# Performance work log

Measured on AMD Instinct MI355X. Metric: run time of the kernel, lower is better.

## Reference

```python
import jax, jax.numpy as jnp
import numpy as np

B, S, H, D = 2, 512, 64, 64   # batch, seq_len, head_dim, d_v=d_k
DT = 0.01                      # uniform measurement time step
NU, DELTA, ETA = 0.5, 1.0, 1.0


def _cmat(k, dout, din, scale):
    kr, ki = jax.random.split(k)
    return jnp.stack([jax.random.normal(kr, (dout, din)),
                      jax.random.normal(ki, (dout, din))]) * scale


def _cmm(W, b, X):
    """Complex matmul + bias. W:(2,O,I), b:(2,O,1), X:(B,2,S,I) -> (B,2,S,O)."""
    Yr = X[:, 0] @ W[0].T - X[:, 1] @ W[1].T + b[0].T
    Yi = X[:, 0] @ W[1].T + X[:, 1] @ W[0].T + b[1].T
    return jnp.stack([Yr, Yi], axis=1)


def _chad(K, V):
    """Complex hadamard of kernel K:(2,Si,Sj,D) with V:(B,2,Sj,D) -> (B,2,Si,Sj,D)."""
    Vr, Vi = V[:, 0, None], V[:, 1, None]           # (B,1,Sj,D)
    return jnp.stack([K[0][None] * Vr - K[1][None] * Vi,
                      K[0][None] * Vi + K[1][None] * Vr], axis=1)


def setup_inputs() -> dict:
    key = jax.random.key(0)
    ks = jax.random.split(key, 20)
    sc = 1.0 / np.sqrt(2 * H)
    t = jnp.arange(S + 1, dtype=jnp.float32) * DT
    return {
        "X_q": jax.random.normal(ks[0], (B, 2, S, H), jnp.float32),
        "X_k": jax.random.normal(ks[1], (B, 2, S, H), jnp.float32),
        "X_v": jax.random.normal(ks[2], (B, 2, S, H), jnp.float32),
        "t_measure_all": jnp.tile(t[None], (B, 1)),
        "lambda1": jnp.stack([jax.random.normal(ks[3], (D // 2, 1)),
                              jax.random.normal(ks[4], (D // 2, 1))]),
        "lam_Omega_sqrt": jax.random.normal(ks[5], (1, D, 1)) / np.sqrt(D),
        "lam_Omega0_sqrt": jax.random.normal(ks[6], (1, D, 1)) / np.sqrt(D),
        "lam_Gamma_sqrt": jax.random.normal(ks[7], (1, D, 1)) / np.sqrt(D),
        "lam_C": jnp.ones((1, D, 1), jnp.float32),
        "W_q": _cmat(ks[8], D, H, sc), "W_k": _cmat(ks[9], D, H, sc),
        "W_v": _cmat(ks[10], D, H, sc), "W_p": _cmat(ks[11], H, D, sc),
        "W_e": _cmat(ks[12], H, D, sc),
        "b_q": _cmat(ks[13], D, 1, sc), "b_k": _cmat(ks[14], D, 1, sc),
        "b_v": _cmat(ks[15], D, 1, sc), "b_p": _cmat(ks[16], H, 1, sc),
        "b_e": _cmat(ks[17], H, 1, sc),
    }


def reference(X_q, X_k, X_v, t_measure_all, lambda1, lam_Omega_sqrt,
              lam_Omega0_sqrt, lam_Gamma_sqrt, lam_C, W_q, W_k, W_v, W_p, W_e,
              b_q, b_k, b_v, b_p, b_e):
    # Stable conjugate-pair eigenvalues lambda_h (real<0) from lambda1 (2, D/2, 1)
    lr = -jnp.abs(lambda1[0, :, 0])
    li = lambda1[1, :, 0]
    real = jnp.concatenate([lr, lr])        # (D,)
    imag = jnp.concatenate([li, -li])       # (D,)
    Om = (lam_Omega_sqrt ** 2)[0, :, 0]
    Om0 = (lam_Omega0_sqrt ** 2)[0, :, 0]
    Gam = (lam_Gamma_sqrt ** 2)[0, :, 0]
    C = lam_C[0, :, 0]

    # Complex QKV projections
    Q = _cmm(W_q, b_q, X_q)
    Kk = _cmm(W_k, b_k, X_k)
    V = _cmm(W_v, b_v, X_v)

    # Pairwise propagation kernel exp(lambda * (t_i - t_j))
    t = t_measure_all[0, :-1]                       # (S,)
    dt = t[:, None] - t[None, :]                    # (S,S)
    decay = jnp.exp(real * dt[:, :, None])
    ph = imag * dt[:, :, None]
    Kexp = jnp.stack([decay * jnp.cos(ph), decay * jnp.sin(ph)])  # (2,S,S,D)

    # Kalman steady-state precision: propagated variance + measurement noise
    exp2 = jnp.exp((2.0 * real) * jnp.abs(dt)[:, :, None])        # (S,S,D)
    var = exp2 * Om0 + Om * (exp2 - 1.0) / (2.0 * real)
    P = 1.0 / (C ** 2 * var + Gam)                                # (S,S,D)

    # Estimates (propagated values) and residuals (query vs propagated key)
    Xhat = _chad(Kexp, V)                           # (B,2,S,S,D)
    Khat = _chad(Kexp, Kk)
    R = Q[:, :, :, None, :] - C * Khat              # (B,2,S,S,D)

    maha = P * (R[:, 0] ** 2 + R[:, 1] ** 2)        # (B,S,S,D)
    denom = 1.0 + NU * jnp.sum(maha, axis=-1, keepdims=True)
    mask = jnp.tril(jnp.ones((S, S), X_q.dtype))[:, :, None]
    A = (P / denom) * mask
    Xhat = Xhat * mask
    Qij = A / jnp.sum(A, axis=2, keepdims=True)     # normalize over j
    est_v = jnp.sum(Qij[:, None] * Xhat, axis=3)    # (B,2,S,D)

    est = _cmm(W_e, b_e, est_v)

    # One-step prediction in eigenbasis
    dtl = t_measure_all[:, -1] - t_measure_all[:, -2]   # (B,)
    dr = jnp.exp(real * dtl[:, None])
    pph = imag * dtl[:, None]
    mr, mi = dr * jnp.cos(pph), dr * jnp.sin(pph)       # (B,D)
    pr = mr[:, None] * est_v[:, 0] - mi[:, None] * est_v[:, 1]
    pi = mr[:, None] * est_v[:, 1] + mi[:, None] * est_v[:, 0]
    pred = _cmm(W_p, b_p, jnp.stack([pr, pi], axis=1))

    out = DELTA * pred + ETA * est
    return (est, out, Qij, Xhat, jnp.stack([real, imag]))
```

## Files before the change

### kernel.cpp

```cpp
#include <hip/hip_runtime.h>
#include <math.h>

#define SQ 512
#define NU_C 0.5f

typedef float fvec4 __attribute__((ext_vector_type(4)));
typedef float fvec2 __attribute__((ext_vector_type(2)));

#define EST_OFF   0
#define OUT_OFF   131072
#define QIJ_OFF   262144
#define XHAT_OFF  33816576
#define LAM_OFF   100925440

#define WQ_OFF  0
#define WK_OFF  131072
#define WV_OFF  262144
#define WEV_OFF 393216

__global__ __launch_bounds__(256) void proj_kernel(
    const float* __restrict__ Xq, const float* __restrict__ Xk, const float* __restrict__ Xv,
    const float* __restrict__ Wq, const float* __restrict__ Wk, const float* __restrict__ Wv,
    const float* __restrict__ bq, const float* __restrict__ bk, const float* __restrict__ bv,
    float* __restrict__ ws)
{
    const int TILE = 16;
    __shared__ float WT0[64 * 65];
    __shared__ float WT1[64 * 65];
    __shared__ float XT[2 * TILE * 64];

    int t   = threadIdx.x;
    int blk = blockIdx.x;
    int p   = blk >> 6;
    int sub = blk & 63;
    int b   = sub >> 5;
    int s0  = (sub & 31) * TILE;

    const float* Xs[3]   = {Xq, Xk, Xv};
    const float* Wsrc[3] = {Wq, Wk, Wv};
    const float* bs[3]   = {bq, bk, bv};
    float* dst[3] = {ws + WQ_OFF, ws + WK_OFF, ws + WV_OFF};

    const float* W = Wsrc[p];
    for (int it = 0; it < 16; ++it) {
        int e = it * 256 + t;
        int dd = e >> 6, hw = e & 63;
        WT0[hw * 65 + dd] = W[e];
        WT1[hw * 65 + dd] = W[4096 + e];
    }
    const float* X = Xs[p];
    for (int it = 0; it < (2 * TILE * 64) / 256; ++it) {
        int e = it * 256 + t;
        int ri = e >> 10;
        int sl = (e >> 6) & (TILE - 1);
        int hw = e & 63;
        XT[e] = X[(size_t)(b * 2 + ri) * (SQ * 64) + (size_t)(s0 + sl) * 64 + hw];
    }
    __syncthreads();

    int dd = t & 63, sg = t >> 6;
    float b0 = bs[p][dd], b1 = bs[p][64 + dd];
    for (int sl = sg; sl < TILE; sl += 4) {
        float ar = b0, ai = b1;
        for (int h = 0; h < 64; ++h) {
            float xr = XT[sl * 64 + h];
            float xi = XT[TILE * 64 + sl * 64 + h];
            float w0 = WT0[h * 65 + dd];
            float w1 = WT1[h * 65 + dd];
            ar += xr * w0 - xi * w1;
            ai += xr * w1 + xi * w0;
        }
        float2 o; o.x = ar; o.y = ai;
        *(float2*)&dst[p][(size_t)((b * SQ + s0 + sl) * 64 + dd) * 2] = o;
    }
}

__global__ __launch_bounds__(512, 4) void main_kernel(
    const float* __restrict__ tm,
    const float* __restrict__ lam1,
    const float* __restrict__ lOm, const float* __restrict__ lOm0,
    const float* __restrict__ lGam, const float* __restrict__ lC,
    const float* __restrict__ ws,
    float* __restrict__ evw,
    float* __restrict__ out)
{
    __shared__ float t_lds[SQ];
    __shared__ float rden_l[2][SQ];
    __shared__ float red[8][2][3][64];
    __shared__ float rs_l[2][64];

    int tid  = threadIdx.x;
    int lane = tid & 63;
    int wave = tid >> 6;
    int q    = lane & 31;
    int h2   = lane >> 5;
    int d0   = 2 * q, d1 = 2 * q + 1;
    int bx = (int)blockIdx.x;
    int i = (bx < 256) ? (SQ - 1 - bx) : (bx - 256);

    float la0 = lam1[d0 & 31], lb0 = lam1[32 + (d0 & 31)];
    float la1 = lam1[d1 & 31], lb1 = lam1[32 + (d1 & 31)];
    float rv0 = -fabsf(la0),  rv1 = -fabsf(la1);
    float iv0 = (d0 < 32) ? lb0 : -lb0;
    float iv1 = (d1 < 32) ? lb1 : -lb1;
    float Om_0 = lOm[d0] * lOm[d0],   Om_1 = lOm[d1] * lOm[d1];
    float Oo_0 = lOm0[d0] * lOm0[d0], Oo_1 = lOm0[d1] * lOm0[d1];
    float Gm_0 = lGam[d0] * lGam[d0], Gm_1 = lGam[d1] * lGam[d1];
    float C_0 = lC[d0], C_1 = lC[d1];
    float r2r0 = 1.0f / (2.0f * rv0), r2r1 = 1.0f / (2.0f * rv1);
    float pA0 = C_0 * C_0 * (Oo_0 + Om_0 * r2r0);
    float pB0 = Gm_0 - C_0 * C_0 * Om_0 * r2r0;
    float pA1 = C_1 * C_1 * (Oo_1 + Om_1 * r2r1);
    float pB1 = Gm_1 - C_1 * C_1 * Om_1 * r2r1;

    for (int s = tid; s < SQ; s += 512) t_lds[s] = tm[s];
    __syncthreads();

    const fvec4* Kw4 = (const fvec4*)(ws + WK_OFF);
    const fvec4* Vw4 = (const fvec4*)(ws + WV_OFF);
    const fvec4* Qw4 = (const fvec4*)(ws + WQ_OFF);

    float ti = t_lds[i];
    fvec4 qb0 = Qw4[(size_t)(0 * SQ + i) * 32 + q];
    fvec4 qb1 = Qw4[(size_t)(1 * SQ + i) * 32 + q];

    float sA00 = 0, sA01 = 0, sXr00 = 0, sXr01 = 0, sXi00 = 0, sXi01 = 0;
    float sA10 = 0, sA11 = 0, sXr10 = 0, sXr11 = 0, sXi10 = 0, sXi11 = 0;

    float* xh0 = out + XHAT_OFF + (size_t)(0 * SQ + i) * SQ * 64;
    float* xh1 = out + XHAT_OFF + (size_t)(1 * SQ + i) * SQ * 64;
    float* xh2 = out + XHAT_OFF + (size_t)(2 * SQ + i) * SQ * 64;
    float* xh3 = out + XHAT_OFF + (size_t)(3 * SQ + i) * SQ * 64;
    float* qij0 = out + QIJ_OFF + (size_t)(0 * SQ + i) * SQ * 64;
    float* qij1 = out + QIJ_OFF + (size_t)(1 * SQ + i) * SQ * 64;

    #pragma unroll 2
    for (int j0 = 2 * wave; j0 <= i; j0 += 16) {
        int j = j0 + h2;
        if (j <= i) {
            float dt = ti - t_lds[j];
            float e_0 = __expf(rv0 * dt);
            float e_1 = __expf(rv1 * dt);
            float s_0, c_0, s_1, c_1;
            __sincosf(iv0 * dt, &s_0, &c_0);
            __sincosf(iv1 * dt, &s_1, &c_1);
            float ar0 = e_0 * c_0, ai0 = e_0 * s_0;
            float ar1 = e_1 * c_1, ai1 = e_1 * s_1;
            float P_0 = 1.0f / fmaf(e_0 * e_0, pA0, pB0);
            float P_1 = 1.0f / fmaf(e_1 * e_1, pA1, pB1);

            fvec4 k0 = Kw4[(size_t)(0 * SQ + j) * 32 + q];
            fvec4 v0 = Vw4[(size_t)(0 * SQ + j) * 32 + q];
            fvec4 k1 = Kw4[(size_t)(1 * SQ + j) * 32 + q];
            fvec4 v1 = Vw4[(size_t)(1 * SQ + j) * 32 + q];

            float xr00 = ar0 * v0[0] - ai0 * v0[1], xi00 = ar0 * v0[1] + ai0 * v0[0];
            float xr01 = ar1 * v0[2] - ai1 * v0[3], xi01 = ar1 * v0[3] + ai1 * v0[2];
            float kr00 = ar0 * k0[0] - ai0 * k0[1], ki00 = ar0 * k0[1] + ai0 * k0[0];
            float kr01 = ar1 * k0[2] - ai1 * k0[3], ki01 = ar1 * k0[3] + ai1 * k0[2];
            float Rr00 = qb0[0] - C_0 * kr00, Ri00 = qb0[1] - C_0 * ki00;
            float Rr01 = qb0[2] - C_1 * kr01, Ri01 = qb0[3] - C_1 * ki01;
            float xr10 = ar0 * v1[0] - ai0 * v1[1], xi10 = ar0 * v1[1] + ai0 * v1[0];
            float xr11 = ar1 * v1[2] - ai1 * v1[3], xi11 = ar1 * v1[3] + ai1 * v1[2];
            float kr10 = ar0 * k1[0] - ai0 * k1[1], ki10 = ar0 * k1[1] + ai0 * k1[0];
            float kr11 = ar1 * k1[2] - ai1 * k1[3], ki11 = ar1 * k1[3] + ai1 * k1[2];
            float Rr10 = qb1[0] - C_0 * kr10, Ri10 = qb1[1] - C_0 * ki10;
            float Rr11 = qb1[2] - C_1 * kr11, Ri11 = qb1[3] - C_1 * ki11;

            float m0 = P_0 * fmaf(Rr00, Rr00, Ri00 * Ri00) + P_1 * fmaf(Rr01, Rr01, Ri01 * Ri01);
            float m1 = P_0 * fmaf(Rr10, Rr10, Ri10 * Ri10) + P_1 * fmaf(Rr11, Rr11, Ri11 * Ri11);
            #pragma unroll
            for (int off = 16; off > 0; off >>= 1) {
                m0 += __shfl_xor(m0, off);
                m1 += __shfl_xor(m1, off);
            }
            float rdb0 = 1.0f / (1.0f + NU_C * m0);
            float rdb1 = 1.0f / (1.0f + NU_C * m1);
            float A00 = P_0 * rdb0, A01 = P_1 * rdb0;
            float A10 = P_0 * rdb1, A11 = P_1 * rdb1;
            sA00 += A00; sXr00 = fmaf(A00, xr00, sXr00); sXi00 = fmaf(A00, xi00, sXi00);
            sA01 += A01; sXr01 = fmaf(A01, xr01, sXr01); sXi01 = fmaf(A01, xi01, sXi01);
            sA10 += A10; sXr10 = fmaf(A10, xr10, sXr10); sXi10 = fmaf(A10, xi10, sXi10);
            sA11 += A11; sXr11 = fmaf(A11, xr11, sXr11); sXi11 = fmaf(A11, xi11, sXi11);

            size_t jb = (size_t)j * 64 + d0;
            fvec2 w0v = {xr00, xr01}; __builtin_nontemporal_store(w0v, (fvec2*)(xh0 + jb));
            fvec2 w1v = {xi00, xi01}; __builtin_nontemporal_store(w1v, (fvec2*)(xh1 + jb));
            fvec2 w2v = {xr10, xr11}; __builtin_nontemporal_store(w2v, (fvec2*)(xh2 + jb));
            fvec2 w3v = {xi10, xi11}; __builtin_nontemporal_store(w3v, (fvec2*)(xh3 + jb));
            if (q == 0) { rden_l[0][j] = rdb0; rden_l[1][j] = rdb1; }
        }
    }

    sA00 += __shfl_xor(sA00, 32); sXr00 += __shfl_xor(sXr00, 32); sXi00 += __shfl_xor(sXi00, 32);
    sA01 += __shfl_xor(sA01, 32); sXr01 += __shfl_xor(sXr01, 32); sXi01 += __shfl_xor(sXi01, 32);
    sA10 += __shfl_xor(sA10, 32); sXr10 += __shfl_xor(sXr10, 32); sXi10 += __shfl_xor(sXi10, 32);
    sA11 += __shfl_xor(sA11, 32); sXr11 += __shfl_xor(sXr11, 32); sXi11 += __shfl_xor(sXi11, 32);
    if (h2 == 0) {
        fvec2 a0 = {sA00, sA01};  *(fvec2*)&red[wave][0][0][d0] = a0;
        fvec2 x0 = {sXr00, sXr01}; *(fvec2*)&red[wave][0][1][d0] = x0;
        fvec2 y0 = {sXi00, sXi01}; *(fvec2*)&red[wave][0][2][d0] = y0;
        fvec2 a1 = {sA10, sA11};  *(fvec2*)&red[wave][1][0][d0] = a1;
        fvec2 x1 = {sXr10, sXr11}; *(fvec2*)&red[wave][1][1][d0] = x1;
        fvec2 y1 = {sXi10, sXi11}; *(fvec2*)&red[wave][1][2][d0] = y1;
    }
    __syncthreads();

    if (wave == 0) {
        int d = lane;
        float tA0 = 0, tXr0 = 0, tXi0 = 0, tA1 = 0, tXr1 = 0, tXi1 = 0;
        #pragma unroll
        for (int w = 0; w < 8; ++w) {
            tA0 += red[w][0][0][d]; tXr0 += red[w][0][1][d]; tXi0 += red[w][0][2][d];
            tA1 += red[w][1][0][d]; tXr1 += red[w][1][1][d]; tXi1 += red[w][1][2][d];
        }
        float rs0 = 1.0f / tA0, rs1 = 1.0f / tA1;
        rs_l[0][d] = rs0; rs_l[1][d] = rs1;
        float2 ev0; ev0.x = tXr0 * rs0; ev0.y = tXi0 * rs0;
        float2 ev1; ev1.x = tXr1 * rs1; ev1.y = tXi1 * rs1;
        *(float2*)&evw[(size_t)((0 * SQ + i) * 64 + d) * 2] = ev0;
        *(float2*)&evw[(size_t)((1 * SQ + i) * 64 + d) * 2] = ev1;
    }
    __syncthreads();

    float rs00 = rs_l[0][d0], rs01 = rs_l[0][d1];
    float rs10 = rs_l[1][d0], rs11 = rs_l[1][d1];

    #pragma unroll 2
    for (int j0 = 2 * wave; j0 <= i; j0 += 16) {
        int j = j0 + h2;
        if (j <= i) {
            float dt = ti - t_lds[j];
            float e2_0 = __expf(2.0f * rv0 * dt);
            float e2_1 = __expf(2.0f * rv1 * dt);
            float P_0 = 1.0f / fmaf(e2_0, pA0, pB0);
            float P_1 = 1.0f / fmaf(e2_1, pA1, pB1);
            float rdb0 = rden_l[0][j];
            float rdb1 = rden_l[1][j];
            size_t jb = (size_t)j * 64 + d0;
            fvec2 q0v = {P_0 * rdb0 * rs00, P_1 * rdb0 * rs01};
            fvec2 q1v = {P_0 * rdb1 * rs10, P_1 * rdb1 * rs11};
            __builtin_nontemporal_store(q0v, (fvec2*)(qij0 + jb));
            __builtin_nontemporal_store(q1v, (fvec2*)(qij1 + jb));
        }
    }

    int nz4 = ((SQ - 1 - i) * 64) >> 2;
    if (nz4 > 0) {
        fvec4 z = {0.f, 0.f, 0.f, 0.f};
        size_t zb = (size_t)(i + 1) * 64;
        float* regs[6] = {qij0 + zb, qij1 + zb, xh0 + zb, xh1 + zb, xh2 + zb, xh3 + zb};
        for (int r6 = 0; r6 < 6; ++r6) {
            float* p4 = regs[r6];
            for (int k4 = tid; k4 < nz4; k4 += 512)
                __builtin_nontemporal_store(z, (fvec4*)(p4 + (size_t)k4 * 4));
        }
    }
}

__global__ __launch_bounds__(256) void epi_kernel(
    const float* __restrict__ tm,
    const float* __restrict__ lam1,
    const float* __restrict__ We, const float* __restrict__ be,
    const float* __restrict__ Wp, const float* __restrict__ bp,
    const float* __restrict__ evw,
    float* __restrict__ out)
{
    const int TILE = 8;
    __shared__ float WT0[64 * 65];
    __shared__ float WT1[64 * 65];
    __shared__ float EVr[TILE * 64];
    __shared__ float EVi[TILE * 64];
    __shared__ float mr_s[64], mi_s[64];

    int t = threadIdx.x;
    int blk = blockIdx.x;
    int b = blk >> 6;
    int s0 = (blk & 63) * TILE;

    if (blk == 0 && t < 128) {
        int dd = t & 63;
        float l0 = lam1[dd & 31];
        float l1 = lam1[32 + (dd & 31)];
        float v = (t < 64) ? -fabsf(l0) : ((dd < 32) ? l1 : -l1);
        out[LAM_OFF + t] = v;
    }
    if (t < 64) {
        int dd = t;
        float l0 = lam1[dd & 31];
        float l1 = lam1[32 + (dd & 31)];
        float realv = -fabsf(l0);
        float imagv = (dd < 32) ? l1 : -l1;
        float dtl = tm[b * (SQ + 1) + SQ] - tm[b * (SQ + 1) + SQ - 1];
        float e = __expf(realv * dtl);
        float s, c; __sincosf(imagv * dtl, &s, &c);
        mr_s[dd] = e * c; mi_s[dd] = e * s;
    }
    {
        const float* src = evw + (size_t)(b * SQ + s0) * 128;
        for (int it = 0; it < (TILE * 128) / 256; ++it) {
            int e = it * 256 + t;
            float v = src[e];
            int sl = e >> 7, dd = (e >> 1) & 63, ri = e & 1;
            if (ri == 0) EVr[sl * 64 + dd] = v; else EVi[sl * 64 + dd] = v;
        }
    }
    for (int it = 0; it < 16; ++it) {
        int e = it * 256 + t;
        int hw = e >> 6, dd = e & 63;
        WT0[dd * 65 + hw] = We[e];
        WT1[dd * 65 + hw] = We[4096 + e];
    }
    __syncthreads();

    int h = t & 63, sg = t >> 6;
    float estr[2], esti[2];
    float be0 = be[h], be1 = be[64 + h];
    #pragma unroll
    for (int k = 0; k < 2; ++k) {
        int sl = sg + k * 4;
        float ar = be0, ai = be1;
        for (int dd = 0; dd < 64; ++dd) {
            float er = EVr[sl * 64 + dd], ei = EVi[sl * 64 + dd];
            float w0 = WT0[dd * 65 + h], w1 = WT1[dd * 65 + h];
            ar += er * w0 - ei * w1;
            ai += er * w1 + ei * w0;
        }
        estr[k] = ar; esti[k] = ai;
        out[EST_OFF + (size_t)((b * 2 + 0) * SQ + s0 + sl) * 64 + h] = ar;
        out[EST_OFF + (size_t)((b * 2 + 1) * SQ + s0 + sl) * 64 + h] = ai;
    }
    __syncthreads();
    for (int it = 0; it < 16; ++it) {
        int e = it * 256 + t;
        int hw = e >> 6, dd = e & 63;
        WT0[dd * 65 + hw] = Wp[e];
        WT1[dd * 65 + hw] = Wp[4096 + e];
    }
    __syncthreads();
    float bp0 = bp[h], bp1 = bp[64 + h];
    #pragma unroll
    for (int k = 0; k < 2; ++k) {
        int sl = sg + k * 4;
        float ar = bp0, ai = bp1;
        for (int dd = 0; dd < 64; ++dd) {
            float er = EVr[sl * 64 + dd], ei = EVi[sl * 64 + dd];
            float pr = mr_s[dd] * er - mi_s[dd] * ei;
            float pi = mr_s[dd] * ei + mi_s[dd] * er;
            float w0 = WT0[dd * 65 + h], w1 = WT1[dd * 65 + h];
            ar += pr * w0 - pi * w1;
            ai += pr * w1 + pi * w0;
        }
        out[OUT_OFF + (size_t)((b * 2 + 0) * SQ + s0 + sl) * 64 + h] = ar + estr[k];
        out[OUT_OFF + (size_t)((b * 2 + 1) * SQ + s0 + sl) * 64 + h] = ai + esti[k];
    }
}

extern "C" void kernel_launch(void* const* d_in, const int* in_sizes, int n_in,
                              void* d_out, int out_size, void* d_ws, size_t ws_size,
                              hipStream_t stream)
{
    const float* Xq   = (const float*)d_in[0];
    const float* Xk   = (const float*)d_in[1];
    const float* Xv   = (const float*)d_in[2];
    const float* tm   = (const float*)d_in[3];
    const float* lam1 = (const float*)d_in[4];
    const float* lOm  = (const float*)d_in[5];
    const float* lOm0 = (const float*)d_in[6];
    const float* lGam = (const float*)d_in[7];
    const float* lC   = (const float*)d_in[8];
    const float* Wq   = (const float*)d_in[9];
    const float* Wk   = (const float*)d_in[10];
    const float* Wv   = (const float*)d_in[11];
    const float* Wp   = (const float*)d_in[12];
    const float* We   = (const float*)d_in[13];
    const float* bq   = (const float*)d_in[14];
    const float* bk   = (const float*)d_in[15];
    const float* bv   = (const float*)d_in[16];
    const float* bp   = (const float*)d_in[17];
    const float* be   = (const float*)d_in[18];
    float* out = (float*)d_out;
    float* ws  = (float*)d_ws;

    proj_kernel<<<192, 256, 0, stream>>>(Xq, Xk, Xv, Wq, Wk, Wv, bq, bk, bv, ws);
    main_kernel<<<512, 512, 0, stream>>>(tm, lam1, lOm, lOm0, lGam, lC, ws, ws + WEV_OFF, out);
    epi_kernel<<<128, 256, 0, stream>>>(tm, lam1, We, be, Wp, bp, ws + WEV_OFF, out);
}
```

Baseline: 112.3 us.

## Split main kernel work across batch, one batch per 256-thread block

The main kernel now launches 1024 blocks of 256 threads, each handling a single (batch, row) pair, where before one 512-thread block handled both batch elements for a row. This halves the per-thread register state and gives more, smaller blocks for load balancing across the triangular workload. The cost is that the exp/sincos kernel terms, which were shared between the two batch elements, are now computed twice, and the time vector is loaded into LDS in twice as many blocks.

```diff
diff --git a/kernel.cpp b/kernel.cpp
--- a/kernel.cpp
+++ b/kernel.cpp
@@ -75,7 +75,7 @@
     }
 }
 
-__global__ __launch_bounds__(512, 4) void main_kernel(
+__global__ __launch_bounds__(256, 4) void main_kernel(
     const float* __restrict__ tm,
     const float* __restrict__ lam1,
     const float* __restrict__ lOm, const float* __restrict__ lOm0,
@@ -85,9 +85,9 @@
     float* __restrict__ out)
 {
     __shared__ float t_lds[SQ];
-    __shared__ float rden_l[2][SQ];
-    __shared__ float red[8][2][3][64];
-    __shared__ float rs_l[2][64];
+    __shared__ float rden_l[SQ];
+    __shared__ float red[4][3][64];
+    __shared__ float rs_l[64];
 
     int tid  = threadIdx.x;
     int lane = tid & 63;
@@ -96,7 +96,9 @@
     int h2   = lane >> 5;
     int d0   = 2 * q, d1 = 2 * q + 1;
     int bx = (int)blockIdx.x;
-    int i = (bx < 256) ? (SQ - 1 - bx) : (bx - 256);
+    int r  = bx >> 1;
+    int b  = bx & 1;
+    int i = (r < 256) ? (SQ - 1 - r) : (r - 256);
 
     float la0 = lam1[d0 & 31], lb0 = lam1[32 + (d0 & 31)];
     float la1 = lam1[d1 & 31], lb1 = lam1[32 + (d1 & 31)];
@@ -113,7 +115,7 @@
     float pA1 = C_1 * C_1 * (Oo_1 + Om_1 * r2r1);
     float pB1 = Gm_1 - C_1 * C_1 * Om_1 * r2r1;
 
-    for (int s = tid; s < SQ; s += 512) t_lds[s] = tm[s];
+    for (int s = tid; s < SQ; s += 256) t_lds[s] = tm[s];
     __syncthreads();
 
     const fvec4* Kw4 = (const fvec4*)(ws + WK_OFF);
@@ -121,21 +123,16 @@
     const fvec4* Qw4 = (const fvec4*)(ws + WQ_OFF);
 
     float ti = t_lds[i];
-    fvec4 qb0 = Qw4[(size_t)(0 * SQ + i) * 32 + q];
-    fvec4 qb1 = Qw4[(size_t)(1 * SQ + i) * 32 + q];
-
-    float sA00 = 0, sA01 = 0, sXr00 = 0, sXr01 = 0, sXi00 = 0, sXi01 = 0;
-    float sA10 = 0, sA11 = 0, sXr10 = 0, sXr11 = 0, sXi10 = 0, sXi11 = 0;
-
-    float* xh0 = out + XHAT_OFF + (size_t)(0 * SQ + i) * SQ * 64;
-    float* xh1 = out + XHAT_OFF + (size_t)(1 * SQ + i) * SQ * 64;
-    float* xh2 = out + XHAT_OFF + (size_t)(2 * SQ + i) * SQ * 64;
-    float* xh3 = out + XHAT_OFF + (size_t)(3 * SQ + i) * SQ * 64;
-    float* qij0 = out + QIJ_OFF + (size_t)(0 * SQ + i) * SQ * 64;
-    float* qij1 = out + QIJ_OFF + (size_t)(1 * SQ + i) * SQ * 64;
+    fvec4 qb = Qw4[(size_t)(b * SQ + i) * 32 + q];
+
+    float sA0 = 0, sA1 = 0, sXr0 = 0, sXr1 = 0, sXi0 = 0, sXi1 = 0;
+
+    float* xhr = out + XHAT_OFF + (size_t)((b * 2 + 0) * SQ + i) * SQ * 64;
+    float* xhi = out + XHAT_OFF + (size_t)((b * 2 + 1) * SQ + i) * SQ * 64;
+    float* qij = out + QIJ_OFF + (size_t)(b * SQ + i) * SQ * 64;
 
     #pragma unroll 2
-    for (int j0 = 2 * wave; j0 <= i; j0 += 16) {
+    for (int j0 = 2 * wave; j0 <= i; j0 += 8) {
         int j = j0 + h2;
         if (j <= i) {
             float dt = ti - t_lds[j];
@@ -149,85 +146,59 @@
             float P_0 = 1.0f / fmaf(e_0 * e_0, pA0, pB0);
             float P_1 = 1.0f / fmaf(e_1 * e_1, pA1, pB1);
 
-            fvec4 k0 = Kw4[(size_t)(0 * SQ + j) * 32 + q];
-            fvec4 v0 = Vw4[(size_t)(0 * SQ + j) * 32 + q];
-            fvec4 k1 = Kw4[(size_t)(1 * SQ + j) * 32 + q];
-            fvec4 v1 = Vw4[(size_t)(1 * SQ + j) * 32 + q];
-
-            float xr00 = ar0 * v0[0] - ai0 * v0[1], xi00 = ar0 * v0[1] + ai0 * v0[0];
-            float xr01 = ar1 * v0[2] - ai1 * v0[3], xi01 = ar1 * v0[3] + ai1 * v0[2];
-            float kr00 = ar0 * k0[0] - ai0 * k0[1], ki00 = ar0 * k0[1] + ai0 * k0[0];
-            float kr01 = ar1 * k0[2] - ai1 * k0[3], ki01 = ar1 * k0[3] + ai1 * k0[2];
-            float Rr00 = qb0[0] - C_0 * kr00, Ri00 = qb0[1] - C_0 * ki00;
-            float Rr01 = qb0[2] - C_1 * kr01, Ri01 = qb0[3] - C_1 * ki01;
-            float xr10 = ar0 * v1[0] - ai0 * v1[1], xi10 = ar0 * v1[1] + ai0 * v1[0];
-            float xr11 = ar1 * v1[2] - ai1 * v1[3], xi11 = ar1 * v1[3] + ai1 * v1[2];
-            float kr10 = ar0 * k1[0] - ai0 * k1[1], ki10 = ar0 * k1[1] + ai0 * k1[0];
-            float kr11 = ar1 * k1[2] - ai1 * k1[3], ki11 = ar1 * k1[3] + ai1 * k1[2];
-            float Rr10 = qb1[0] - C_0 * kr10, Ri10 = qb1[1] - C_0 * ki10;
-            float Rr11 = qb1[2] - C_1 * kr11, Ri11 = qb1[3] - C_1 * ki11;
-
-            float m0 = P_0 * fmaf(Rr00, Rr00, Ri00 * Ri00) + P_1 * fmaf(Rr01, Rr01, Ri01 * Ri01);
-            float m1 = P_0 * fmaf(Rr10, Rr10, Ri10 * Ri10) + P_1 * fmaf(Rr11, Rr11, Ri11 * Ri11);
+            fvec4 k = Kw4[(size_t)(b * SQ + j) * 32 + q];
+            fvec4 v = Vw4[(size_t)(b * SQ + j) * 32 + q];
+
+            float xr0 = ar0 * v[0] - ai0 * v[1], xi0 = ar0 * v[1] + ai0 * v[0];
+            float xr1 = ar1 * v[2] - ai1 * v[3], xi1 = ar1 * v[3] + ai1 * v[2];
+            float kr0 = ar0 * k[0] - ai0 * k[1], ki0 = ar0 * k[1] + ai0 * k[0];
+            float kr1 = ar1 * k[2] - ai1 * k[3], ki1 = ar1 * k[3] + ai1 * k[2];
+            float Rr0 = qb[0] - C_0 * kr0, Ri0 = qb[1] - C_0 * ki0;
+            float Rr1 = qb[2] - C_1 * kr1, Ri1 = qb[3] - C_1 * ki1;
+
+            float m = P_0 * fmaf(Rr0, Rr0, Ri0 * Ri0) + P_1 * fmaf(Rr1, Rr1, Ri1 * Ri1);
             #pragma unroll
-            for (int off = 16; off > 0; off >>= 1) {
-                m0 += __shfl_xor(m0, off);
-                m1 += __shfl_xor(m1, off);
-            }
-            float rdb0 = 1.0f / (1.0f + NU_C * m0);
-            float rdb1 = 1.0f / (1.0f + NU_C * m1);
-            float A00 = P_0 * rdb0, A01 = P_1 * rdb0;
-            float A10 = P_0 * rdb1, A11 = P_1 * rdb1;
-            sA00 += A00; sXr00 = fmaf(A00, xr00, sXr00); sXi00 = fmaf(A00, xi00, sXi00);
-            sA01 += A01; sXr01 = fmaf(A01, xr01, sXr01); sXi01 = fmaf(A01, xi01, sXi01);
-            sA10 += A10; sXr10 = fmaf(A10, xr10, sXr10); sXi10 = fmaf(A10, xi10, sXi10);
-            sA11 += A11; sXr11 = fmaf(A11, xr11, sXr11); sXi11 = fmaf(A11, xi11, sXi11);
+            for (int off = 16; off > 0; off >>= 1)
+                m += __shfl_xor(m, off);
+            float rdb = 1.0f / (1.0f + NU_C * m);
+            float A0 = P_0 * rdb, A1 = P_1 * rdb;
+            sA0 += A0; sXr0 = fmaf(A0, xr0, sXr0); sXi0 = fmaf(A0, xi0, sXi0);
+            sA1 += A1; sXr1 = fmaf(A1, xr1, sXr1); sXi1 = fmaf(A1, xi1, sXi1);
 
             size_t jb = (size_t)j * 64 + d0;
-            fvec2 w0v = {xr00, xr01}; __builtin_nontemporal_store(w0v, (fvec2*)(xh0 + jb));
-            fvec2 w1v = {xi00, xi01}; __builtin_nontemporal_store(w1v, (fvec2*)(xh1 + jb));
-            fvec2 w2v = {xr10, xr11}; __builtin_nontemporal_store(w2v, (fvec2*)(xh2 + jb));
-            fvec2 w3v = {xi10, xi11}; __builtin_nontemporal_store(w3v, (fvec2*)(xh3 + jb));
-            if (q == 0) { rden_l[0][j] = rdb0; rden_l[1][j] = rdb1; }
-        }
-    }
-
-    sA00 += __shfl_xor(sA00, 32); sXr00 += __shfl_xor(sXr00, 32); sXi00 += __shfl_xor(sXi00, 32);
-    sA01 += __shfl_xor(sA01, 32); sXr01 += __shfl_xor(sXr01, 32); sXi01 += __shfl_xor(sXi01, 32);
-    sA10 += __shfl_xor(sA10, 32); sXr10 += __shfl_xor(sXr10, 32); sXi10 += __shfl_xor(sXi10, 32);
-    sA11 += __shfl_xor(sA11, 32); sXr11 += __shfl_xor(sXr11, 32); sXi11 += __shfl_xor(sXi11, 32);
+            fvec2 wr = {xr0, xr1}; __builtin_nontemporal_store(wr, (fvec2*)(xhr + jb));
+            fvec2 wi = {xi0, xi1}; __builtin_nontemporal_store(wi, (fvec2*)(xhi + jb));
+            if (q == 0) rden_l[j] = rdb;
+        }
+    }
+
+    sA0 += __shfl_xor(sA0, 32); sXr0 += __shfl_xor(sXr0, 32); sXi0 += __shfl_xor(sXi0, 32);
+    sA1 += __shfl_xor(sA1, 32); sXr1 += __shfl_xor(sXr1, 32); sXi1 += __shfl_xor(sXi1, 32);
     if (h2 == 0) {
-        fvec2 a0 = {sA00, sA01};  *(fvec2*)&red[wave][0][0][d0] = a0;
-        fvec2 x0 = {sXr00, sXr01}; *(fvec2*)&red[wave][0][1][d0] = x0;
-        fvec2 y0 = {sXi00, sXi01}; *(fvec2*)&red[wave][0][2][d0] = y0;
-        fvec2 a1 = {sA10, sA11};  *(fvec2*)&red[wave][1][0][d0] = a1;
-        fvec2 x1 = {sXr10, sXr11}; *(fvec2*)&red[wave][1][1][d0] = x1;
-        fvec2 y1 = {sXi10, sXi11}; *(fvec2*)&red[wave][1][2][d0] = y1;
+        fvec2 a = {sA0, sA1};   *(fvec2*)&red[wave][0][d0] = a;
+        fvec2 x = {sXr0, sXr1}; *(fvec2*)&red[wave][1][d0] = x;
+        fvec2 y = {sXi0, sXi1}; *(fvec2*)&red[wave][2][d0] = y;
     }
     __syncthreads();
 
     if (wave == 0) {
         int d = lane;
-        float tA0 = 0, tXr0 = 0, tXi0 = 0, tA1 = 0, tXr1 = 0, tXi1 = 0;
+        float tA = 0, tXr = 0, tXi = 0;
         #pragma unroll
-        for (int w = 0; w < 8; ++w) {
-            tA0 += red[w][0][0][d]; tXr0 += red[w][0][1][d]; tXi0 += red[w][0][2][d];
-            tA1 += red[w][1][0][d]; tXr1 += red[w][1][1][d]; tXi1 += red[w][1][2][d];
-        }
-        float rs0 = 1.0f / tA0, rs1 = 1.0f / tA1;
-        rs_l[0][d] = rs0; rs_l[1][d] = rs1;
-        float2 ev0; ev0.x = tXr0 * rs0; ev0.y = tXi0 * rs0;
-        float2 ev1; ev1.x = tXr1 * rs1; ev1.y = tXi1 * rs1;
-        *(float2*)&evw[(size_t)((0 * SQ + i) * 64 + d) * 2] = ev0;
-        *(float2*)&evw[(size_t)((1 * SQ + i) * 64 + d) * 2] = ev1;
-    }
-    __syncthreads();
-
-    float rs00 = rs_l[0][d0], rs01 = rs_l[0][d1];
-    float rs10 = rs_l[1][d0], rs11 = rs_l[1][d1];
+        for (int w = 0; w < 4; ++w) {
+            tA += red[w][0][d]; tXr += red[w][1][d]; tXi += red[w][2][d];
+        }
+        float rs = 1.0f / tA;
+        rs_l[d] = rs;
+        float2 ev; ev.x = tXr * rs; ev.y = tXi * rs;
+        *(float2*)&evw[(size_t)((b * SQ + i) * 64 + d) * 2] = ev;
+    }
+    __syncthreads();
+
+    float rs0 = rs_l[d0], rs1 = rs_l[d1];
 
     #pragma unroll 2
-    for (int j0 = 2 * wave; j0 <= i; j0 += 16) {
+    for (int j0 = 2 * wave; j0 <= i; j0 += 8) {
         int j = j0 + h2;
         if (j <= i) {
             float dt = ti - t_lds[j];
@@ -235,13 +206,10 @@
             float e2_1 = __expf(2.0f * rv1 * dt);
             float P_0 = 1.0f / fmaf(e2_0, pA0, pB0);
             float P_1 = 1.0f / fmaf(e2_1, pA1, pB1);
-            float rdb0 = rden_l[0][j];
-            float rdb1 = rden_l[1][j];
+            float rdb = rden_l[j];
             size_t jb = (size_t)j * 64 + d0;
-            fvec2 q0v = {P_0 * rdb0 * rs00, P_1 * rdb0 * rs01};
-            fvec2 q1v = {P_0 * rdb1 * rs10, P_1 * rdb1 * rs11};
-            __builtin_nontemporal_store(q0v, (fvec2*)(qij0 + jb));
-            __builtin_nontemporal_store(q1v, (fvec2*)(qij1 + jb));
+            fvec2 qv = {P_0 * rdb * rs0, P_1 * rdb * rs1};
+            __builtin_nontemporal_store(qv, (fvec2*)(qij + jb));
         }
     }
 
@@ -249,10 +217,10 @@
     if (nz4 > 0) {
         fvec4 z = {0.f, 0.f, 0.f, 0.f};
         size_t zb = (size_t)(i + 1) * 64;
-        float* regs[6] = {qij0 + zb, qij1 + zb, xh0 + zb, xh1 + zb, xh2 + zb, xh3 + zb};
-        for (int r6 = 0; r6 < 6; ++r6) {
-            float* p4 = regs[r6];
-            for (int k4 = tid; k4 < nz4; k4 += 512)
+        float* regs[3] = {qij + zb, xhr + zb, xhi + zb};
+        for (int r3 = 0; r3 < 3; ++r3) {
+            float* p4 = regs[r3];
+            for (int k4 = tid; k4 < nz4; k4 += 256)
                 __builtin_nontemporal_store(z, (fvec4*)(p4 + (size_t)k4 * 4));
         }
     }
@@ -383,6 +351,6 @@
     float* ws  = (float*)d_ws;
 
     proj_kernel<<<192, 256, 0, stream>>>(Xq, Xk, Xv, Wq, Wk, Wv, bq, bk, bv, ws);
-    main_kernel<<<512, 512, 0, stream>>>(tm, lam1, lOm, lOm0, lGam, lC, ws, ws + WEV_OFF, out);
+    main_kernel<<<1024, 256, 0, stream>>>(tm, lam1, lOm, lOm0, lGam, lC, ws, ws + WEV_OFF, out);
     epi_kernel<<<128, 256, 0, stream>>>(tm, lam1, We, be, Wp, bp, ws + WEV_OFF, out);
 }
```

Result: slower. 115.1 us (+2.5%).

## Split Xhat output writing into separate balanced kernel

Applied to the files above, without the earlier changes.

Moves the Xhat tensor writes, both the lower-triangle values and the zero fill, out of the main attention kernel into a new kernel. The new kernel has one block per (row, batch) pair and a uniform workload. This removes the row-length load imbalance for the largest output and leaves the Qij kernel writing less. In exchange it recomputes the exp/sincos propagation factors and rereads V, and adds a kernel launch.

```diff
diff --git a/kernel.cpp b/kernel.cpp
--- a/kernel.cpp
+++ b/kernel.cpp
@@ -75,7 +75,58 @@
     }
 }
 
-__global__ __launch_bounds__(512, 4) void main_kernel(
+__global__ __launch_bounds__(256, 4) void xhat_kernel(
+    const float* __restrict__ tm,
+    const float* __restrict__ lam1,
+    const float* __restrict__ ws,
+    float* __restrict__ out)
+{
+    __shared__ float t_lds[SQ];
+    int t = threadIdx.x;
+    int q = t & 31, jslot = t >> 5;
+    int d0 = 2 * q, d1 = 2 * q + 1;
+    int bx = (int)blockIdx.x;
+    int i = bx >> 1, b = bx & 1;
+
+    float la0 = lam1[d0 & 31], lb0 = lam1[32 + (d0 & 31)];
+    float la1 = lam1[d1 & 31], lb1 = lam1[32 + (d1 & 31)];
+    float rv0 = -fabsf(la0), rv1 = -fabsf(la1);
+    float iv0 = (d0 < 32) ? lb0 : -lb0;
+    float iv1 = (d1 < 32) ? lb1 : -lb1;
+
+    for (int s = t; s < SQ; s += 256) t_lds[s] = tm[s];
+    __syncthreads();
+
+    const fvec4* Vw4 = (const fvec4*)(ws + WV_OFF);
+    float ti = t_lds[i];
+    float* xhr = out + XHAT_OFF + (size_t)((b * 2 + 0) * SQ + i) * SQ * 64;
+    float* xhi = out + XHAT_OFF + (size_t)((b * 2 + 1) * SQ + i) * SQ * 64;
+
+    #pragma unroll 2
+    for (int j = jslot; j < SQ; j += 8) {
+        size_t jb = (size_t)j * 64 + d0;
+        if (j <= i) {
+            float dt = ti - t_lds[j];
+            float e0 = __expf(rv0 * dt), e1 = __expf(rv1 * dt);
+            float s0, c0, s1, c1;
+            __sincosf(iv0 * dt, &s0, &c0);
+            __sincosf(iv1 * dt, &s1, &c1);
+            float ar0 = e0 * c0, ai0 = e0 * s0;
+            float ar1 = e1 * c1, ai1 = e1 * s1;
+            fvec4 v = Vw4[(size_t)(b * SQ + j) * 32 + q];
+            fvec2 wr = {ar0 * v[0] - ai0 * v[1], ar1 * v[2] - ai1 * v[3]};
+            fvec2 wi = {ar0 * v[1] + ai0 * v[0], ar1 * v[3] + ai1 * v[2]};
+            __builtin_nontemporal_store(wr, (fvec2*)(xhr + jb));
+            __builtin_nontemporal_store(wi, (fvec2*)(xhi + jb));
+        } else {
+            fvec2 z = {0.f, 0.f};
+            __builtin_nontemporal_store(z, (fvec2*)(xhr + jb));
+            __builtin_nontemporal_store(z, (fvec2*)(xhi + jb));
+        }
+    }
+}
+
+__global__ __launch_bounds__(512, 4) void qij_kernel(
     const float* __restrict__ tm,
     const float* __restrict__ lam1,
     const float* __restrict__ lOm, const float* __restrict__ lOm0,
@@ -127,10 +178,6 @@
     float sA00 = 0, sA01 = 0, sXr00 = 0, sXr01 = 0, sXi00 = 0, sXi01 = 0;
     float sA10 = 0, sA11 = 0, sXr10 = 0, sXr11 = 0, sXi10 = 0, sXi11 = 0;
 
-    float* xh0 = out + XHAT_OFF + (size_t)(0 * SQ + i) * SQ * 64;
-    float* xh1 = out + XHAT_OFF + (size_t)(1 * SQ + i) * SQ * 64;
-    float* xh2 = out + XHAT_OFF + (size_t)(2 * SQ + i) * SQ * 64;
-    float* xh3 = out + XHAT_OFF + (size_t)(3 * SQ + i) * SQ * 64;
     float* qij0 = out + QIJ_OFF + (size_t)(0 * SQ + i) * SQ * 64;
     float* qij1 = out + QIJ_OFF + (size_t)(1 * SQ + i) * SQ * 64;
 
@@ -183,11 +230,6 @@
             sA10 += A10; sXr10 = fmaf(A10, xr10, sXr10); sXi10 = fmaf(A10, xi10, sXi10);
             sA11 += A11; sXr11 = fmaf(A11, xr11, sXr11); sXi11 = fmaf(A11, xi11, sXi11);
 
-            size_t jb = (size_t)j * 64 + d0;
-            fvec2 w0v = {xr00, xr01}; __builtin_nontemporal_store(w0v, (fvec2*)(xh0 + jb));
-            fvec2 w1v = {xi00, xi01}; __builtin_nontemporal_store(w1v, (fvec2*)(xh1 + jb));
-            fvec2 w2v = {xr10, xr11}; __builtin_nontemporal_store(w2v, (fvec2*)(xh2 + jb));
-            fvec2 w3v = {xi10, xi11}; __builtin_nontemporal_store(w3v, (fvec2*)(xh3 + jb));
             if (q == 0) { rden_l[0][j] = rdb0; rden_l[1][j] = rdb1; }
         }
     }
@@ -249,9 +291,9 @@
     if (nz4 > 0) {
         fvec4 z = {0.f, 0.f, 0.f, 0.f};
         size_t zb = (size_t)(i + 1) * 64;
-        float* regs[6] = {qij0 + zb, qij1 + zb, xh0 + zb, xh1 + zb, xh2 + zb, xh3 + zb};
-        for (int r6 = 0; r6 < 6; ++r6) {
-            float* p4 = regs[r6];
+        float* regs[2] = {qij0 + zb, qij1 + zb};
+        for (int r2 = 0; r2 < 2; ++r2) {
+            float* p4 = regs[r2];
             for (int k4 = tid; k4 < nz4; k4 += 512)
                 __builtin_nontemporal_store(z, (fvec4*)(p4 + (size_t)k4 * 4));
         }
@@ -383,6 +425,7 @@
     float* ws  = (float*)d_ws;
 
     proj_kernel<<<192, 256, 0, stream>>>(Xq, Xk, Xv, Wq, Wk, Wv, bq, bk, bv, ws);
-    main_kernel<<<512, 512, 0, stream>>>(tm, lam1, lOm, lOm0, lGam, lC, ws, ws + WEV_OFF, out);
+    xhat_kernel<<<1024, 256, 0, stream>>>(tm, lam1, ws, out);
+    qij_kernel<<<512, 512, 0, stream>>>(tm, lam1, lOm, lOm0, lGam, lC, ws, ws + WEV_OFF, out);
     epi_kernel<<<128, 256, 0, stream>>>(tm, lam1, We, be, Wp, bp, ws + WEV_OFF, out);
 }
```

Measured after the change: 128.7 us. 14.7% more time.
